# Optimization experiments

Hardware: AMD Instinct MI355X
Metric: run time of the kernel (lower is better)

The kernel has to match this reference:

```python
import jax, jax.numpy as jnp
import numpy as np

P_LEN, Q_LEN, BATCH, D, H = 300, 50, 32, 256, 256


def _make_params(key):
    ks = jax.random.split(key, 6)
    s = lambda k, shape, fan: jax.random.normal(k, shape, jnp.float32) * (1.0 / np.sqrt(fan))
    return dict(
        Wq=s(ks[0], (2, H, D), D), bq=jnp.zeros((2, H), jnp.float32),
        Wp=s(ks[1], (2, H, D), D), bp=jnp.zeros((2, H), jnp.float32),
        Wr=s(ks[2], (2, H, H), H), br=jnp.zeros((2, H), jnp.float32),
        Wg=s(ks[3], (2, H), H), bg=jnp.zeros((2,), jnp.float32),
        ln_g=jnp.ones((2, 2 * D), jnp.float32), ln_b=jnp.zeros((2, 2 * D), jnp.float32),
        W_ih=s(ks[4], (2, 4 * H, 2 * D), 2 * D), W_hh=s(ks[5], (2, 4 * H, H), H),
        b_ih=jnp.zeros((2, 4 * H), jnp.float32), b_hh=jnp.zeros((2, 4 * H), jnp.float32),
    )


def setup_inputs() -> dict:
    key = jax.random.key(0)
    k1, k2, k3, k4, kp = jax.random.split(key, 5)
    content_vec = jax.random.normal(k1, (P_LEN, BATCH, D), jnp.float32)
    question_vec = jax.random.normal(k2, (Q_LEN, BATCH, D), jnp.float32)
    p_len = jax.random.randint(k3, (BATCH,), P_LEN // 2, P_LEN + 1)
    q_len = jax.random.randint(k4, (BATCH,), Q_LEN // 2, Q_LEN + 1)
    content_mask = (jnp.arange(P_LEN)[None, :] < p_len[:, None]).astype(jnp.int32)
    question_mask = (jnp.arange(Q_LEN)[None, :] < q_len[:, None]).astype(jnp.int32)
    inp = dict(content_vec=content_vec, content_mask=content_mask,
               question_vec=question_vec, question_mask=question_mask)
    inp.update(_make_params(kp))
    return inp


def _masked_flip(v, mask):
    # v: (P, B, D); mask: (B, P). Reverses the valid prefix of each sequence,
    # leaving padding positions in place (standard Match-LSTM masked_flip).
    P = v.shape[0]
    lengths = mask.sum(axis=1)  # (B,)
    t = jnp.arange(P)[:, None]  # (P, 1)
    idx = jnp.where(t < lengths[None, :], lengths[None, :] - 1 - t, t)  # (P, B)
    idx = jnp.broadcast_to(idx[:, :, None], v.shape)
    return jnp.take_along_axis(v, idx, axis=0)


def _uni_match(cv, qv, qmask, Wq, bq, Wp, bp, Wr, br, Wg, bg, ln_g, ln_b, W_ih, W_hh, b_ih, b_hh):
    # cv: (P, B, D), qv: (Q, B, D), qmask: (B, Q)
    B = cv.shape[1]
    Hh = Wr.shape[0]
    wh = jnp.einsum('qbd,hd->qbh', qv, Wq) + bq      # (Q, B, H), precomputed once
    hp_all = jnp.einsum('pbd,hd->pbh', cv, Wp) + bp  # (P, B, H), precomputed
    pad = (qmask == 0)                               # (B, Q)

    def step(carry, xs):
        h, c = carry
        cv_t, hp_t = xs
        hr = h @ Wr.T + br                                    # (B, H)
        g = jnp.tanh(wh + hp_t[None] + hr[None])              # (Q, B, H)
        alpha = (jnp.einsum('qbh,h->qb', g, Wg) + bg).T       # (B, Q)
        alpha = jax.nn.softmax(jnp.where(pad, -jnp.inf, alpha), axis=1)
        h_alpha = jnp.einsum('bq,qbd->bd', alpha, qv)         # (B, D)
        z = jnp.concatenate([cv_t, h_alpha], axis=1)          # (B, 2D)
        mu = jnp.mean(z, axis=-1, keepdims=True)
        var = jnp.mean((z - mu) ** 2, axis=-1, keepdims=True)
        z = (z - mu) * jax.lax.rsqrt(var + 1e-5) * ln_g + ln_b
        gates = z @ W_ih.T + b_ih + h @ W_hh.T + b_hh         # (B, 4H)
        i_, f_, g_, o_ = jnp.split(gates, 4, axis=1)          # torch LSTMCell order i,f,g,o
        c_n = jax.nn.sigmoid(f_) * c + jax.nn.sigmoid(i_) * jnp.tanh(g_)
        h_n = jax.nn.sigmoid(o_) * jnp.tanh(c_n)
        return (h_n, c_n), h_n

    h0 = jnp.zeros((B, Hh), cv.dtype)
    _, hs = jax.lax.scan(step, (h0, h0), (cv, hp_all))
    return hs  # (P, B, H)


def reference(content_vec, content_mask, question_vec, question_mask,
              Wq, bq, Wp, bp, Wr, br, Wg, bg, ln_g, ln_b, W_ih, W_hh, b_ih, b_hh):
    # Dropout with p=0 (inference) is identity.
    args = lambda i: (Wq[i], bq[i], Wp[i], bp[i], Wr[i], br[i], Wg[i], bg[i],
                      ln_g[i], ln_b[i], W_ih[i], W_hh[i], b_ih[i], b_hh[i])
    right = _uni_match(content_vec, question_vec, question_mask, *args(0))
    cv_flip = _masked_flip(content_vec, content_mask)
    left = _uni_match(cv_flip, question_vec, question_mask, *args(1))
    left = _masked_flip(left, content_mask)
    res = jnp.concatenate([right, left], axis=2)            # (P, B, 2H)
    return content_mask.T[:, :, None].astype(res.dtype) * res
```

## Files before the change

kernel.cpp:

```cpp
#include <hip/hip_runtime.h>
#include <hip/hip_fp16.h>

typedef unsigned int u32;
typedef unsigned long long u64;
typedef _Float16 half2_t __attribute__((ext_vector_type(2)));
typedef _Float16 f16x8 __attribute__((ext_vector_type(8)));
typedef float f32x16 __attribute__((ext_vector_type(16)));

static constexpr int PL = 300;
static constexpr int QL = 50;
static constexpr int B  = 32;
static constexpr int D  = 256;
static constexpr int H  = 256;

__device__ __forceinline__ float fdot2(u32 w, u32 x, float acc) {
    return __builtin_amdgcn_fdot2(__builtin_bit_cast(half2_t, w),
                                  __builtin_bit_cast(half2_t, x), acc, false);
}
__device__ __forceinline__ u32 packh2(float a, float b) {
    half2_t h2; h2[0] = (_Float16)a; h2[1] = (_Float16)b;
    return __builtin_bit_cast(u32, h2);
}
__device__ __forceinline__ f32x16 mfma16(uint4 a, uint4 b, f32x16 c) {
    return __builtin_amdgcn_mfma_f32_32x32x16_f16(
        __builtin_bit_cast(f16x8, a), __builtin_bit_cast(f16x8, b), c, 0, 0, 0);
}
__device__ __forceinline__ u32 a_ld32(const u32* p) {
    return __hip_atomic_load(p, __ATOMIC_RELAXED, __HIP_MEMORY_SCOPE_AGENT);
}
__device__ __forceinline__ u64 a_ld64(const u64* p) {
    return __hip_atomic_load(p, __ATOMIC_RELAXED, __HIP_MEMORY_SCOPE_AGENT);
}
__device__ __forceinline__ void a_st32(u32* p, u32 v) {
    __hip_atomic_store(p, v, __ATOMIC_RELAXED, __HIP_MEMORY_SCOPE_AGENT);
}
__device__ __forceinline__ void a_st64(u64* p, u64 v) {
    __hip_atomic_store(p, v, __ATOMIC_RELAXED, __HIP_MEMORY_SCOPE_AGENT);
}

__global__ __launch_bounds__(256) void pack_wt(const float* __restrict__ Wih,
                                               const float* __restrict__ Whh,
                                               const float* __restrict__ Wr,
                                               const float* __restrict__ lng,
                                               u32* __restrict__ dst) {
    int id = blockIdx.x * 256 + threadIdx.x;
    int u = id & 255;
    int rw = (id >> 8) % 40;
    int j  = ((id >> 8) / 40) % 32;
    int dd = (id >> 8) / 1280;
    float a = 0.f, c = 0.f;
    if (rw < 32) {
        int R = (rw >> 3) * 256 + 8 * j + (rw & 7);
        if (u < 128) {
            int k = 2 * u;
            a = Wih[((size_t)dd * 1024 + R) * 512 + k]     * lng[dd * 512 + k];
            c = Wih[((size_t)dd * 1024 + R) * 512 + k + 1] * lng[dd * 512 + k + 1];
        } else {
            int k = 2 * (u - 128);
            a = Whh[((size_t)dd * 1024 + R) * 256 + k];
            c = Whh[((size_t)dd * 1024 + R) * 256 + k + 1];
        }
    } else if (u >= 128) {
        int k = 2 * (u - 128);
        int wrr = 8 * j + (rw - 32);
        a = Wr[((size_t)dd * 256 + wrr) * 256 + k];
        c = Wr[((size_t)dd * 256 + wrr) * 256 + k + 1];
    }
    dst[id] = packh2(a, c);
}

__global__ __launch_bounds__(256) void prep_proj(const float* __restrict__ X,
                                                 const float* __restrict__ W,
                                                 const float* __restrict__ Bv,
                                                 __half* __restrict__ out,
                                                 int T, int nt) {
    int id = blockIdx.x;
    int tb = id % nt; id /= nt;
    int b  = id % B;  id /= B;
    int g  = id;
    int t0 = tb * 8;
    int nr = T - t0; if (nr > 8) nr = 8;
    __shared__ __align__(16) float xs[8][256];
    int tid = threadIdx.x;
    for (int r = 0; r < nr; r++) xs[r][tid] = X[((t0 + r) * B + b) * D + tid];
    __syncthreads();
    const float4* wrow = (const float4*)&W[(g * H + tid) * D];
    float bb = Bv[g * H + tid];
    float acc[8];
#pragma unroll
    for (int r = 0; r < 8; r++) acc[r] = bb;
    for (int d4 = 0; d4 < D / 4; d4++) {
        float4 w = wrow[d4];
#pragma unroll
        for (int r = 0; r < 8; r++) {
            float4 x = *(const float4*)&xs[r][d4 * 4];
            acc[r] = fmaf(w.x, x.x, fmaf(w.y, x.y, fmaf(w.z, x.z, fmaf(w.w, x.w, acc[r]))));
        }
    }
    for (int r = 0; r < nr; r++)
        out[((g * B + b) * T + t0 + r) * H + tid] = __float2half(acc[r]);
}

__global__ __launch_bounds__(256) void vp_prep(const float* __restrict__ qv,
                                               const float* __restrict__ Wih,
                                               const float* __restrict__ lng,
                                               __half* __restrict__ VP) {
    int blk = blockIdx.x;
    int dd = blk >> 8, b = (blk >> 3) & 31, rc = blk & 7;
    __shared__ __align__(16) u32 qg[50 * 128];
    __shared__ __align__(16) u32 wch[128 * 128];
    int tid = threadIdx.x;
    for (int v = tid; v < 6400; v += 256) {
        int q = v >> 7, i = v & 127;
        float a = qv[((size_t)q * 32 + b) * 256 + 2 * i]     * lng[dd * 512 + 256 + 2 * i];
        float c = qv[((size_t)q * 32 + b) * 256 + 2 * i + 1] * lng[dd * 512 + 256 + 2 * i + 1];
        qg[v] = packh2(a, c);
    }
    for (int v = tid; v < 16384; v += 256) {
        int rl = v >> 7, i = v & 127;
        int r = rc * 128 + rl;
        float a = Wih[((size_t)dd * 1024 + r) * 512 + 256 + 2 * i];
        float c = Wih[((size_t)dd * 1024 + r) * 512 + 256 + 2 * i + 1];
        wch[v] = packh2(a, c);
    }
    __syncthreads();
    for (int p = tid; p < 128 * 56; p += 256) {
        int rl = p / 56, q = p % 56;
        int r = rc * 128 + rl;
        float acc = 0.f;
        if (q < 50) {
            const u32* qr = qg + q * 128;
            const u32* wr = wch + rl * 128;
#pragma unroll 8
            for (int i = 0; i < 128; i++) acc = fdot2(wr[i], qr[i], acc);
        }
        VP[((size_t)(dd * 32 + b) * 1024 + r) * 56 + q] = __float2half(acc);
    }
}

__global__ __launch_bounds__(256) void gram_prep(const float* __restrict__ qv,
                                                 float* __restrict__ G,
                                                 float* __restrict__ qs) {
    int b = blockIdx.x;
    __shared__ float qvs[50 * 256];
    int tid = threadIdx.x;
    for (int v = tid; v < 12800; v += 256) {
        int q = v >> 8, k = v & 255;
        qvs[v] = qv[((size_t)q * 32 + b) * 256 + k];
    }
    __syncthreads();
    for (int p = tid; p < 2500; p += 256) {
        int q = p / 50, q2 = p % 50;
        float acc = 0.f;
        for (int k = 0; k < 256; k++) acc = fmaf(qvs[q * 256 + k], qvs[q2 * 256 + k], acc);
        G[((size_t)b * 50 + q) * 50 + q2] = acc;
    }
    if (tid < 52) {
        float s = 0.f;
        if (tid < 50) for (int k = 0; k < 256; k++) s += qvs[tid * 256 + k];
        qs[b * 52 + tid] = s;
    }
}

__global__ __launch_bounds__(256) void cvstats_prep(const float* __restrict__ cv,
                                                    float* __restrict__ st) {
    int blk = blockIdx.x;
    int t = blk >> 5, b = blk & 31;
    int tid = threadIdx.x;
    float v = cv[((size_t)t * 32 + b) * 256 + tid];
    float s = v, s2 = v * v;
#pragma unroll
    for (int m = 32; m; m >>= 1) { s += __shfl_xor(s, m, 64); s2 += __shfl_xor(s2, m, 64); }
    __shared__ float red[8];
    if ((tid & 63) == 0) { red[(tid >> 6) * 2] = s; red[(tid >> 6) * 2 + 1] = s2; }
    __syncthreads();
    if (tid == 0) {
        float S = red[0] + red[2] + red[4] + red[6];
        float S2 = red[1] + red[3] + red[5] + red[7];
        st[((size_t)b * 300 + t) * 2] = S;
        st[((size_t)b * 300 + t) * 2 + 1] = S2;
    }
}

__global__ __launch_bounds__(256) void c1c2_prep(const float* __restrict__ Wih,
                                                 const float* __restrict__ lng,
                                                 const float* __restrict__ lnb,
                                                 const float* __restrict__ bih,
                                                 const float* __restrict__ bhh,
                                                 float* __restrict__ C12) {
    int id = blockIdx.x * 256 + threadIdx.x;
    int dd = id >> 10, R = id & 1023;
    float s1 = 0.f, s2 = 0.f;
    const float* wr = &Wih[((size_t)dd * 1024 + R) * 512];
    for (int k = 0; k < 512; k++) {
        float w = wr[k];
        s1 = fmaf(w, lng[dd * 512 + k], s1);
        s2 = fmaf(w, lnb[dd * 512 + k], s2);
    }
    C12[(size_t)id * 2] = s1;
    C12[(size_t)id * 2 + 1] = s2 + bih[dd * 1024 + R] + bhh[dd * 1024 + R];
}

__global__ __launch_bounds__(256, 1) void scan6(
    const float* __restrict__ cv,
    const int*   __restrict__ cmask,
    const int*   __restrict__ qmask,
    const float* __restrict__ Wgv,
    const float* __restrict__ bgv,
    const float* __restrict__ brp,
    const u32*   __restrict__ Wtp,
    const __half* __restrict__ whp,
    const __half* __restrict__ hpp,
    const __half* __restrict__ VP,
    const float* __restrict__ C12,
    const float* __restrict__ G,
    const float* __restrict__ qsr,
    const float* __restrict__ cvst,
    u32* __restrict__ exch_h,
    u32* __restrict__ B1ex,
    u32* __restrict__ B2ex,
    u32* __restrict__ B3ex,
    u32* __restrict__ tags,
    float* __restrict__ out)
{
    int blk = blockIdx.x;
    int dd = blk >> 5, j = blk & 31;
    int tid = threadIdx.x;
    int lane = tid & 63, wave = tid >> 6;
    int rr = lane & 31, kh = lane >> 5, sw = rr & 7;

    __shared__ __align__(16) u32 sh_wt[40 * 256];
    __shared__ __align__(16) u32 sh_x[32 * 256];
    __shared__ __align__(16) u32 sh_wh[6400];
    __shared__ float sh_G[50 * 50];
    __shared__ float sh_red1[2 * 32 * 33];
    __shared__ float sh_red2[2 * 32 * 33];
    __shared__ float sh_red3[4 * 32 * 8];
    __shared__ float sh_C1[1024];
    __shared__ float sh_C2[1024];
    __shared__ float sh_a[256];
    __shared__ float sh_qs[52];
    __shared__ float sh_af[64];
    __shared__ __align__(16) u32 sh_al2[28];
    __shared__ float sh_alpha[64];
    __shared__ float sh_qb[64];
    __shared__ float sh_r2[4];
    __shared__ float sh_cs[2];
    __shared__ int   sh_len[32];

    for (int v = tid; v < 40 * 256; v += 256) {
        int rl = v >> 8, u = v & 255;
        int c4 = u >> 2, w = u & 3;
        sh_wt[rl * 256 + (((c4 ^ (rl & 7)) << 2) | w)] =
            Wtp[((size_t)(dd * 32 + j) * 40 + rl) * 256 + u];
    }
    {
        const u32* whsrc = (const u32*)(whp + (size_t)(dd * 32 + j) * QL * H);
        for (int i = tid; i < 6400; i += 256) sh_wh[i] = whsrc[i];
    }
    for (int v = tid; v < 2500; v += 256) sh_G[v] = G[(size_t)j * 2500 + v];
    if (tid < 52) sh_qs[tid] = qsr[j * 52 + tid];
    for (int v = tid; v < 1024; v += 256) {
        sh_C1[v] = C12[((size_t)dd * 1024 + v) * 2];
        sh_C2[v] = C12[((size_t)dd * 1024 + v) * 2 + 1];
    }
    if (tid < 64) sh_qb[tid] = (tid < QL) ? (qmask[j * QL + tid] ? 0.f : -1e30f) : -1e30f;
    if (tid < 32) sh_len[tid] = 0;
    __syncthreads();
    {
        int b = tid & 31, part = tid >> 5;
        int t0 = part * 38, t1 = t0 + 38 > PL ? PL : t0 + 38;
        int s = 0;
        for (int tt = t0; tt < t1; tt++) s += cmask[b * PL + tt];
        atomicAdd(&sh_len[b], s);
    }
    __syncthreads();

    float wgr[4];
#pragma unroll
    for (int i = 0; i < 4; i++) wgr[i] = Wgv[dd * H + lane + 64 * i];
    float bgs = bgv[dd];
    float brv = brp[dd * H + tid];
    int len_j = sh_len[j];
    float c_reg = 0.f;

    for (int t = len_j; t < PL; t++)
        out[((size_t)t * B + j) * 512 + dd * 256 + tid] = 0.f;

    if (tid < 128) a_st32(exch_h + (size_t)(dd * 32 + j) * 128 + tid, 0u);
    asm volatile("s_waitcnt vmcnt(0)" ::: "memory");
    __syncthreads();
    if (tid == 0) a_st32(tags + dd * 32 + j, 1u);

    const __half* hpb = hpp + (size_t)(dd * 32 + j) * PL * H;
    const u32* VPu = (const u32*)VP;
    const u32* xrow  = sh_x + rr * 256;
    const u32* wrow  = sh_wt + rr * 256;
    const u32* wrow2 = sh_wt + (8 + rr) * 256;

    for (int t = 0; t < PL; t++) {
        int tsj = dd ? (t < len_j ? len_j - 1 - t : t) : t;

        {
            int b = tid >> 3, sub = tid & 7;
            int lenb = sh_len[b];
            int tsb = dd ? (t < lenb ? lenb - 1 - t : t) : t;
            const float4* src = (const float4*)(cv + ((size_t)tsb * 32 + b) * 256 + sub * 32);
#pragma unroll
            for (int i = 0; i < 4; i++) {
                float4 e = src[2 * i], o = src[2 * i + 1];
                uint4 pk = { packh2(e.x, e.y), packh2(e.z, e.w),
                             packh2(o.x, o.y), packh2(o.z, o.w) };
                int c4 = sub * 4 + i;
                *(uint4*)(sh_x + b * 256 + ((c4 ^ (b & 7)) << 2)) = pk;
            }
        }
        float hpv = __half2float(hpb[(size_t)tsj * H + tid]);
        if (tid == 0) {
            sh_cs[0] = cvst[((size_t)j * 300 + tsj) * 2];
            sh_cs[1] = cvst[((size_t)j * 300 + tsj) * 2 + 1];
        }

        if (wave == 0) {
            for (;;) {
                u32 v = a_ld32(tags + dd * 32 + (lane & 31));
                if (__all(v >= (u32)(t + 1))) break;
                __builtin_amdgcn_s_sleep(1);
            }
        }
        __syncthreads();

#pragma unroll
        for (int m = 0; m < 4; m++) {
            int f4 = m * 256 + tid;
            int b = f4 >> 5, c4h = f4 & 31;
            const u64* s = (const u64*)(exch_h + (size_t)(dd * 32 + b) * 128 + c4h * 4);
            u64 lo = a_ld64(s), hi = a_ld64(s + 1);
            int oct = 32 + c4h;
            u32* dstp = sh_x + b * 256 + ((oct ^ (b & 7)) << 2);
            *(u64*)dstp = lo; *(u64*)(dstp + 2) = hi;
        }
        __syncthreads();

        {
            f32x16 acc1 = {}, acc2 = {};
#pragma unroll
            for (int kk = 0; kk < 8; kk++) {
                int c4 = wave * 16 + 2 * kk + kh;
                int pc4 = (c4 ^ sw) << 2;
                uint4 au = *(const uint4*)(xrow + pc4);
                uint4 bu = *(const uint4*)(wrow + pc4);
                acc1 = mfma16(au, bu, acc1);
            }
#pragma unroll
            for (int kk = 0; kk < 4; kk++) {
                int c4 = 32 + wave * 8 + 2 * kk + kh;
                int pc4 = (c4 ^ sw) << 2;
                uint4 au = *(const uint4*)(xrow + pc4);
                uint4 bu = *(const uint4*)(wrow2 + pc4);
                acc2 = mfma16(au, bu, acc2);
            }
            float* dstP = (wave < 2) ? &sh_red1[wave * 32 * 33] : &sh_red2[(wave - 2) * 32 * 33];
#pragma unroll
            for (int q = 0; q < 16; q++) {
                int b = (q & 3) + 8 * (q >> 2) + 4 * kh;
                dstP[b * 33 + rr] = acc1[q];
            }
            if (rr >= 24) {
#pragma unroll
                for (int q = 0; q < 16; q++) {
                    int b = (q & 3) + 8 * (q >> 2) + 4 * kh;
                    sh_red3[(wave * 32 + b) * 8 + (rr - 24)] = acc2[q];
                }
            }
        }
        __syncthreads();

        {
            int b = tid >> 3, rq = (tid & 7) * 4;
            size_t base = ((size_t)(dd * 32 + b) * 32 + j) * 32 + rq;
            float2 p0, p1;
            p0.x = sh_red1[b * 33 + rq]     + sh_red1[1056 + b * 33 + rq];
            p0.y = sh_red1[b * 33 + rq + 1] + sh_red1[1056 + b * 33 + rq + 1];
            p1.x = sh_red1[b * 33 + rq + 2] + sh_red1[1056 + b * 33 + rq + 2];
            p1.y = sh_red1[b * 33 + rq + 3] + sh_red1[1056 + b * 33 + rq + 3];
            a_st64((u64*)(B1ex + base),     __builtin_bit_cast(u64, p0));
            a_st64((u64*)(B1ex + base) + 1, __builtin_bit_cast(u64, p1));
            p0.x = sh_red2[b * 33 + rq]     + sh_red2[1056 + b * 33 + rq];
            p0.y = sh_red2[b * 33 + rq + 1] + sh_red2[1056 + b * 33 + rq + 1];
            p1.x = sh_red2[b * 33 + rq + 2] + sh_red2[1056 + b * 33 + rq + 2];
            p1.y = sh_red2[b * 33 + rq + 3] + sh_red2[1056 + b * 33 + rq + 3];
            a_st64((u64*)(B2ex + base),     __builtin_bit_cast(u64, p0));
            a_st64((u64*)(B2ex + base) + 1, __builtin_bit_cast(u64, p1));
            int rw = tid & 7;
            float b3 = sh_red3[b * 8 + rw] + sh_red3[(32 + b) * 8 + rw]
                     + sh_red3[(64 + b) * 8 + rw] + sh_red3[(96 + b) * 8 + rw];
            a_st32(B3ex + ((size_t)(dd * 32 + b) * 32 + j) * 8 + rw,
                   __builtin_bit_cast(u32, b3));
        }
        asm volatile("s_waitcnt vmcnt(0)" ::: "memory");
        __syncthreads();
        if (tid == 0) a_st32(tags + 64 + dd * 32 + j, (u32)(t + 1));

        uint4 vp[28];
#pragma unroll
        for (int k = 0; k < 4; k++) {
            const uint4* vr = (const uint4*)(VPu + ((size_t)(dd * 32 + j) * 1024 + k * 256 + tid) * 28);
#pragma unroll
            for (int i = 0; i < 7; i++) vp[k * 7 + i] = vr[i];
        }

        if (wave == 0) {
            for (;;) {
                u32 v = a_ld32(tags + 64 + dd * 32 + (lane & 31));
                if (__all(v >= (u32)(t + 1))) break;
                __builtin_amdgcn_s_sleep(1);
            }
        }
        __syncthreads();

        float bg1[4], bg2[4];
        {
            float hrv = __builtin_bit_cast(float,
                a_ld32(B3ex + ((size_t)(dd * 32 + j) * 32 + (tid >> 3)) * 8 + (tid & 7)));
            sh_a[tid] = hrv + brv + hpv;
#pragma unroll
            for (int k = 0; k < 4; k++) {
                size_t idx = ((size_t)(dd * 32 + j) * 32 + (tid >> 3)) * 32 + k * 8 + (tid & 7);
                bg1[k] = __builtin_bit_cast(float, a_ld32(B1ex + idx));
                bg2[k] = __builtin_bit_cast(float, a_ld32(B2ex + idx));
            }
        }
        __syncthreads();

        {
            float av[4];
#pragma unroll
            for (int i = 0; i < 4; i++) av[i] = sh_a[lane + 64 * i];
            const __half* wh16 = (const __half*)sh_wh;
            for (int q = wave; q < QL; q += 4) {
                float a = 0.f;
#pragma unroll
                for (int i = 0; i < 4; i++) {
                    float xx = (float)wh16[q * 256 + lane + 64 * i] + av[i];
                    float e = __expf(2.f * xx);
                    a = fmaf(wgr[i], (e - 1.f) / (e + 1.f), a);
                }
#pragma unroll
                for (int m = 32; m; m >>= 1) a += __shfl_xor(a, m, 64);
                if (lane == 0) sh_alpha[q] = a + bgs + sh_qb[q];
            }
        }
        __syncthreads();
        if (wave == 0) {
            float v = (lane < QL) ? sh_alpha[lane] : -1e30f;
            float m = v;
#pragma unroll
            for (int s = 32; s; s >>= 1) m = fmaxf(m, __shfl_xor(m, s, 64));
            float e = (lane < QL) ? __expf(v - m) : 0.f;
            float sum = e;
#pragma unroll
            for (int s = 32; s; s >>= 1) sum += __shfl_xor(sum, s, 64);
            float al = (lane < QL) ? e / sum : 0.f;
            sh_af[lane] = al;
            float alo = __shfl_xor(al, 1, 64);
            if (!(lane & 1) && lane < 56) sh_al2[lane >> 1] = packh2(al, alo);
        }
        __syncthreads();

        if (wave == 0) {
            float gd = 0.f;
            if (lane < QL) {
                const float* Grow = sh_G + lane * 50;
                float aq = sh_af[lane];
                for (int q2 = 0; q2 < QL; q2++) gd = fmaf(Grow[q2], sh_af[q2], gd);
                gd *= aq;
            }
#pragma unroll
            for (int m = 32; m; m >>= 1) gd += __shfl_xor(gd, m, 64);
            if (lane == 0) sh_r2[0] = gd;
        } else if (wave == 1) {
            float s = (lane < QL) ? sh_af[lane] * sh_qs[lane] : 0.f;
#pragma unroll
            for (int m = 32; m; m >>= 1) s += __shfl_xor(s, m, 64);
            if (lane == 0) sh_r2[1] = s;
        }
        __syncthreads();

        float aVP[4];
#pragma unroll
        for (int k = 0; k < 4; k++) {
            float acc = 0.f;
#pragma unroll
            for (int i = 0; i < 7; i++) {
                acc = fdot2(vp[k * 7 + i].x, sh_al2[i * 4 + 0], acc);
                acc = fdot2(vp[k * 7 + i].y, sh_al2[i * 4 + 1], acc);
                acc = fdot2(vp[k * 7 + i].z, sh_al2[i * 4 + 2], acc);
                acc = fdot2(vp[k * 7 + i].w, sh_al2[i * 4 + 3], acc);
            }
            aVP[k] = acc;
        }

        float hv;
        {
            float mu = (sh_cs[0] + sh_r2[1]) * (1.f / 512.f);
            float E2 = (sh_cs[1] + sh_r2[0]) * (1.f / 512.f);
            float rs = rsqrtf(E2 - mu * mu + 1e-5f);
            float gk[4];
#pragma unroll
            for (int k = 0; k < 4; k++)
                gk[k] = rs * (bg1[k] + aVP[k]) - rs * mu * sh_C1[k * 256 + tid]
                      + sh_C2[k * 256 + tid] + bg2[k];
            float si = 1.f / (1.f + __expf(-gk[0]));
            float sf = 1.f / (1.f + __expf(-gk[1]));
            float so = 1.f / (1.f + __expf(-gk[3]));
            float eg = __expf(2.f * gk[2]); float tg = (eg - 1.f) / (eg + 1.f);
            float c = sf * c_reg + si * tg;
            float ec = __expf(2.f * c); float tc = (ec - 1.f) / (ec + 1.f);
            hv = so * tc;
            c_reg = c;
            float ho = __shfl_xor(hv, 1, 64);
            if (!(tid & 1))
                a_st32(exch_h + (size_t)(dd * 32 + j) * 128 + (tid >> 1), packh2(hv, ho));
        }
        asm volatile("s_waitcnt vmcnt(0)" ::: "memory");
        __syncthreads();
        if (tid == 0) a_st32(tags + dd * 32 + j, (u32)(t + 2));

        if (t < len_j)
            out[((size_t)tsj * B + j) * 512 + dd * 256 + tid] = hv;
    }
}

extern "C" void kernel_launch(void* const* d_in, const int* in_sizes, int n_in,
                              void* d_out, int out_size, void* d_ws, size_t ws_size,
                              hipStream_t stream) {
    const float* cv    = (const float*)d_in[0];
    const int*   cmask = (const int*)  d_in[1];
    const float* qv    = (const float*)d_in[2];
    const int*   qmask = (const int*)  d_in[3];
    const float* Wq    = (const float*)d_in[4];
    const float* bq    = (const float*)d_in[5];
    const float* Wp    = (const float*)d_in[6];
    const float* bp    = (const float*)d_in[7];
    const float* Wr    = (const float*)d_in[8];
    const float* br    = (const float*)d_in[9];
    const float* Wg    = (const float*)d_in[10];
    const float* bg    = (const float*)d_in[11];
    const float* ln_g  = (const float*)d_in[12];
    const float* ln_b  = (const float*)d_in[13];
    const float* Wih   = (const float*)d_in[14];
    const float* Whh   = (const float*)d_in[15];
    const float* b_ih  = (const float*)d_in[16];
    const float* b_hh  = (const float*)d_in[17];
    float* out = (float*)d_out;

    uint8_t* ws = (uint8_t*)d_ws;
    u32*    Wtp = (u32*)ws;      ws += (size_t)2 * 32 * 40 * 256 * 4;
    __half* VP  = (__half*)ws;   ws += (size_t)2 * 32 * 1024 * 56 * 2;
    __half* whp = (__half*)ws;   ws += (size_t)2 * 32 * 50 * 256 * 2;
    __half* hpp = (__half*)ws;   ws += (size_t)2 * 32 * 300 * 256 * 2;
    float*  C12 = (float*)ws;    ws += (size_t)2 * 1024 * 2 * 4;
    float*  G   = (float*)ws;    ws += (size_t)32 * 50 * 50 * 4;
    float*  qs  = (float*)ws;    ws += (size_t)32 * 52 * 4;
    float*  cvs = (float*)ws;    ws += (size_t)32 * 300 * 2 * 4;
    u32* exch_h = (u32*)ws;      ws += (size_t)64 * 128 * 4;
    u32* B1ex   = (u32*)ws;      ws += (size_t)2 * 32 * 32 * 32 * 4;
    u32* B2ex   = (u32*)ws;      ws += (size_t)2 * 32 * 32 * 32 * 4;
    u32* B3ex   = (u32*)ws;      ws += (size_t)2 * 32 * 32 * 8 * 4;
    u32* tags   = (u32*)ws;

    hipMemsetAsync(tags, 0, 128 * 4, stream);
    hipLaunchKernelGGL(pack_wt, dim3(2560), dim3(256), 0, stream, Wih, Whh, Wr, ln_g, Wtp);
    hipLaunchKernelGGL(prep_proj, dim3(2 * 32 * 7), dim3(256), 0, stream,
                       qv, Wq, bq, whp, QL, 7);
    hipLaunchKernelGGL(prep_proj, dim3(2 * 32 * 38), dim3(256), 0, stream,
                       cv, Wp, bp, hpp, PL, 38);
    hipLaunchKernelGGL(vp_prep, dim3(512), dim3(256), 0, stream, qv, Wih, ln_g, VP);
    hipLaunchKernelGGL(gram_prep, dim3(32), dim3(256), 0, stream, qv, G, qs);
    hipLaunchKernelGGL(cvstats_prep, dim3(9600), dim3(256), 0, stream, cv, cvs);
    hipLaunchKernelGGL(c1c2_prep, dim3(8), dim3(256), 0, stream,
                       Wih, ln_g, ln_b, b_ih, b_hh, C12);
    hipLaunchKernelGGL(scan6, dim3(64), dim3(256), 0, stream,
                       cv, cmask, qmask, Wg, bg, br, Wtp, whp, hpp, VP, C12, G, qs, cvs,
                       exch_h, B1ex, B2ex, B3ex, tags, out);
}
```

Baseline: 4.995 ms.

## Replace flag-based inter-block barriers with sequence-tagged 64-bit exchange words

The per-step cross-block exchange of hidden state and partial reductions now packs a step sequence number into the upper 32 bits of every 64-bit word. Consumers spin on each word individually instead of waiting on a separate tag array. This removes the vmcnt drains, extra __syncthreads and tag publish/poll round-trips from each of the 300 recurrent steps. In exchange, exchange traffic doubles in size and each thread issues many spinning atomic loads, which adds memory traffic and polling cost.

```diff
diff --git a/kernel.cpp b/kernel.cpp
--- a/kernel.cpp
+++ b/kernel.cpp
@@ -25,17 +25,19 @@
     return __builtin_amdgcn_mfma_f32_32x32x16_f16(
         __builtin_bit_cast(f16x8, a), __builtin_bit_cast(f16x8, b), c, 0, 0, 0);
 }
-__device__ __forceinline__ u32 a_ld32(const u32* p) {
-    return __hip_atomic_load(p, __ATOMIC_RELAXED, __HIP_MEMORY_SCOPE_AGENT);
-}
 __device__ __forceinline__ u64 a_ld64(const u64* p) {
     return __hip_atomic_load(p, __ATOMIC_RELAXED, __HIP_MEMORY_SCOPE_AGENT);
 }
-__device__ __forceinline__ void a_st32(u32* p, u32 v) {
-    __hip_atomic_store(p, v, __ATOMIC_RELAXED, __HIP_MEMORY_SCOPE_AGENT);
-}
 __device__ __forceinline__ void a_st64(u64* p, u64 v) {
     __hip_atomic_store(p, v, __ATOMIC_RELAXED, __HIP_MEMORY_SCOPE_AGENT);
+}
+__device__ __forceinline__ u32 spin_word(const u64* p, u32 want) {
+    u64 w = a_ld64(p);
+    while ((u32)(w >> 32) != want) {
+        __builtin_amdgcn_s_sleep(1);
+        w = a_ld64(p);
+    }
+    return (u32)w;
 }
 
 __global__ __launch_bounds__(256) void pack_wt(const float* __restrict__ Wih,
@@ -201,7 +203,7 @@
     C12[(size_t)id * 2 + 1] = s2 + bih[dd * 1024 + R] + bhh[dd * 1024 + R];
 }
 
-__global__ __launch_bounds__(256, 1) void scan6(
+__global__ __launch_bounds__(256, 1) void scan8(
     const float* __restrict__ cv,
     const int*   __restrict__ cmask,
     const int*   __restrict__ qmask,
@@ -216,11 +218,10 @@
     const float* __restrict__ G,
     const float* __restrict__ qsr,
     const float* __restrict__ cvst,
-    u32* __restrict__ exch_h,
-    u32* __restrict__ B1ex,
-    u32* __restrict__ B2ex,
-    u32* __restrict__ B3ex,
-    u32* __restrict__ tags,
+    u64* __restrict__ HX,
+    u64* __restrict__ B1X,
+    u64* __restrict__ B2X,
+    u64* __restrict__ B3X,
     float* __restrict__ out)
 {
     int blk = blockIdx.x;
@@ -287,10 +288,7 @@
     for (int t = len_j; t < PL; t++)
         out[((size_t)t * B + j) * 512 + dd * 256 + tid] = 0.f;
 
-    if (tid < 128) a_st32(exch_h + (size_t)(dd * 32 + j) * 128 + tid, 0u);
-    asm volatile("s_waitcnt vmcnt(0)" ::: "memory");
-    __syncthreads();
-    if (tid == 0) a_st32(tags + dd * 32 + j, 1u);
+    if (tid < 128) a_st64(HX + (size_t)(dd * 32 + j) * 128 + tid, ((u64)1 << 32));
 
     const __half* hpb = hpp + (size_t)(dd * 32 + j) * PL * H;
     const u32* VPu = (const u32*)VP;
@@ -299,7 +297,9 @@
     const u32* wrow2 = sh_wt + (8 + rr) * 256;
 
     for (int t = 0; t < PL; t++) {
+        u32 want = (u32)(t + 1);
         int tsj = dd ? (t < len_j ? len_j - 1 - t : t) : t;
+        __syncthreads();
 
         {
             int b = tid >> 3, sub = tid & 7;
@@ -321,24 +321,13 @@
             sh_cs[1] = cvst[((size_t)j * 300 + tsj) * 2 + 1];
         }
 
-        if (wave == 0) {
-            for (;;) {
-                u32 v = a_ld32(tags + dd * 32 + (lane & 31));
-                if (__all(v >= (u32)(t + 1))) break;
-                __builtin_amdgcn_s_sleep(1);
-            }
-        }
-        __syncthreads();
-
-#pragma unroll
-        for (int m = 0; m < 4; m++) {
-            int f4 = m * 256 + tid;
-            int b = f4 >> 5, c4h = f4 & 31;
-            const u64* s = (const u64*)(exch_h + (size_t)(dd * 32 + b) * 128 + c4h * 4);
-            u64 lo = a_ld64(s), hi = a_ld64(s + 1);
-            int oct = 32 + c4h;
-            u32* dstp = sh_x + b * 256 + ((oct ^ (b & 7)) << 2);
-            *(u64*)dstp = lo; *(u64*)(dstp + 2) = hi;
+#pragma unroll
+        for (int m = 0; m < 16; m++) {
+            int f = m * 256 + tid;
+            int b = f >> 7, c2 = f & 127;
+            u32 pay = spin_word(HX + (size_t)(dd * 32 + b) * 128 + c2, want);
+            int oct = 32 + (c2 >> 2);
+            sh_x[b * 256 + (((oct ^ (b & 7)) << 2) | (c2 & 3))] = pay;
         }
         __syncthreads();
 
@@ -378,29 +367,21 @@
 
         {
             int b = tid >> 3, rq = (tid & 7) * 4;
-            size_t base = ((size_t)(dd * 32 + b) * 32 + j) * 32 + rq;
-            float2 p0, p1;
-            p0.x = sh_red1[b * 33 + rq]     + sh_red1[1056 + b * 33 + rq];
-            p0.y = sh_red1[b * 33 + rq + 1] + sh_red1[1056 + b * 33 + rq + 1];
-            p1.x = sh_red1[b * 33 + rq + 2] + sh_red1[1056 + b * 33 + rq + 2];
-            p1.y = sh_red1[b * 33 + rq + 3] + sh_red1[1056 + b * 33 + rq + 3];
-            a_st64((u64*)(B1ex + base),     __builtin_bit_cast(u64, p0));
-            a_st64((u64*)(B1ex + base) + 1, __builtin_bit_cast(u64, p1));
-            p0.x = sh_red2[b * 33 + rq]     + sh_red2[1056 + b * 33 + rq];
-            p0.y = sh_red2[b * 33 + rq + 1] + sh_red2[1056 + b * 33 + rq + 1];
-            p1.x = sh_red2[b * 33 + rq + 2] + sh_red2[1056 + b * 33 + rq + 2];
-            p1.y = sh_red2[b * 33 + rq + 3] + sh_red2[1056 + b * 33 + rq + 3];
-            a_st64((u64*)(B2ex + base),     __builtin_bit_cast(u64, p0));
-            a_st64((u64*)(B2ex + base) + 1, __builtin_bit_cast(u64, p1));
+            u64 sq = ((u64)want) << 32;
+            size_t base = (size_t)(dd * 32 + b) * 1024 + j * 32 + rq;
+#pragma unroll
+            for (int i = 0; i < 4; i++) {
+                float f1 = sh_red1[b * 33 + rq + i] + sh_red1[1056 + b * 33 + rq + i];
+                float f2 = sh_red2[b * 33 + rq + i] + sh_red2[1056 + b * 33 + rq + i];
+                a_st64(B1X + base + i, sq | (u64)__builtin_bit_cast(u32, f1));
+                a_st64(B2X + base + i, sq | (u64)__builtin_bit_cast(u32, f2));
+            }
             int rw = tid & 7;
             float b3 = sh_red3[b * 8 + rw] + sh_red3[(32 + b) * 8 + rw]
                      + sh_red3[(64 + b) * 8 + rw] + sh_red3[(96 + b) * 8 + rw];
-            a_st32(B3ex + ((size_t)(dd * 32 + b) * 32 + j) * 8 + rw,
-                   __builtin_bit_cast(u32, b3));
-        }
-        asm volatile("s_waitcnt vmcnt(0)" ::: "memory");
-        __syncthreads();
-        if (tid == 0) a_st32(tags + 64 + dd * 32 + j, (u32)(t + 1));
+            a_st64(B3X + (size_t)(dd * 32 + b) * 256 + 8 * j + rw,
+                   sq | (u64)__builtin_bit_cast(u32, b3));
+        }
 
         uint4 vp[28];
 #pragma unroll
@@ -410,26 +391,17 @@
             for (int i = 0; i < 7; i++) vp[k * 7 + i] = vr[i];
         }
 
-        if (wave == 0) {
-            for (;;) {
-                u32 v = a_ld32(tags + 64 + dd * 32 + (lane & 31));
-                if (__all(v >= (u32)(t + 1))) break;
-                __builtin_amdgcn_s_sleep(1);
-            }
-        }
-        __syncthreads();
-
         float bg1[4], bg2[4];
         {
+            size_t bb = (size_t)(dd * 32 + j) * 1024 + (tid >> 3) * 32 + (tid & 7);
+#pragma unroll
+            for (int k = 0; k < 4; k++) {
+                bg1[k] = __builtin_bit_cast(float, spin_word(B1X + bb + k * 8, want));
+                bg2[k] = __builtin_bit_cast(float, spin_word(B2X + bb + k * 8, want));
+            }
             float hrv = __builtin_bit_cast(float,
-                a_ld32(B3ex + ((size_t)(dd * 32 + j) * 32 + (tid >> 3)) * 8 + (tid & 7)));
+                spin_word(B3X + (size_t)(dd * 32 + j) * 256 + tid, want));
             sh_a[tid] = hrv + brv + hpv;
-#pragma unroll
-            for (int k = 0; k < 4; k++) {
-                size_t idx = ((size_t)(dd * 32 + j) * 32 + (tid >> 3)) * 32 + k * 8 + (tid & 7);
-                bg1[k] = __builtin_bit_cast(float, a_ld32(B1ex + idx));
-                bg2[k] = __builtin_bit_cast(float, a_ld32(B2ex + idx));
-            }
         }
         __syncthreads();
 
@@ -521,11 +493,9 @@
             c_reg = c;
             float ho = __shfl_xor(hv, 1, 64);
             if (!(tid & 1))
-                a_st32(exch_h + (size_t)(dd * 32 + j) * 128 + (tid >> 1), packh2(hv, ho));
-        }
-        asm volatile("s_waitcnt vmcnt(0)" ::: "memory");
-        __syncthreads();
-        if (tid == 0) a_st32(tags + dd * 32 + j, (u32)(t + 2));
+                a_st64(HX + (size_t)(dd * 32 + j) * 128 + (tid >> 1),
+                       (((u64)(t + 2)) << 32) | (u64)packh2(hv, ho));
+        }
 
         if (t < len_j)
             out[((size_t)tsj * B + j) * 512 + dd * 256 + tid] = hv;
@@ -564,13 +534,13 @@
     float*  G   = (float*)ws;    ws += (size_t)32 * 50 * 50 * 4;
     float*  qs  = (float*)ws;    ws += (size_t)32 * 52 * 4;
     float*  cvs = (float*)ws;    ws += (size_t)32 * 300 * 2 * 4;
-    u32* exch_h = (u32*)ws;      ws += (size_t)64 * 128 * 4;
-    u32* B1ex   = (u32*)ws;      ws += (size_t)2 * 32 * 32 * 32 * 4;
-    u32* B2ex   = (u32*)ws;      ws += (size_t)2 * 32 * 32 * 32 * 4;
-    u32* B3ex   = (u32*)ws;      ws += (size_t)2 * 32 * 32 * 8 * 4;
-    u32* tags   = (u32*)ws;
-
-    hipMemsetAsync(tags, 0, 128 * 4, stream);
+    u64* HX  = (u64*)ws;         ws += (size_t)2 * 32 * 128 * 8;
+    u64* B1X = (u64*)ws;         ws += (size_t)2 * 32 * 1024 * 8;
+    u64* B2X = (u64*)ws;         ws += (size_t)2 * 32 * 1024 * 8;
+    u64* B3X = (u64*)ws;         ws += (size_t)2 * 32 * 256 * 8;
+
+    hipMemsetAsync(HX, 0, (size_t)(2 * 32 * 128 + 2 * 2 * 32 * 1024 + 2 * 32 * 256) * 8,
+                   stream);
     hipLaunchKernelGGL(pack_wt, dim3(2560), dim3(256), 0, stream, Wih, Whh, Wr, ln_g, Wtp);
     hipLaunchKernelGGL(prep_proj, dim3(2 * 32 * 7), dim3(256), 0, stream,
                        qv, Wq, bq, whp, QL, 7);
@@ -581,7 +551,7 @@
     hipLaunchKernelGGL(cvstats_prep, dim3(9600), dim3(256), 0, stream, cv, cvs);
     hipLaunchKernelGGL(c1c2_prep, dim3(8), dim3(256), 0, stream,
                        Wih, ln_g, ln_b, b_ih, b_hh, C12);
-    hipLaunchKernelGGL(scan6, dim3(64), dim3(256), 0, stream,
+    hipLaunchKernelGGL(scan8, dim3(64), dim3(256), 0, stream,
                        cv, cmask, qmask, Wg, bg, br, Wtp, whp, hpp, VP, C12, G, qs, cvs,
-                       exch_h, B1ex, B2ex, B3ex, tags, out);
-}
+                       HX, B1X, B2X, B3X, out);
+}
```

Result: slower. 5.831 ms (+16.7%).
